# Kernel optimization log

Measured on AMD Instinct MI355X. Metric: run time of the kernel, lower is better.

## Reference

```python
import jax, jax.numpy as jnp
import numpy as np

GROUPS = 16
GROUP_SIZE = 16
K = 3
KK = K * K
BN_EPS = 1e-5


def setup_inputs() -> dict:
    key = jax.random.key(0)
    ks = jax.random.split(key, 6)
    B, C, H, W = 16, 256, 56, 56
    mid = C // 4  # rd_ratio = 4
    x = jax.random.normal(ks[0], (B, C, H, W), dtype=jnp.float32)
    w1 = jax.random.normal(ks[1], (mid, C), dtype=jnp.float32) * (1.0 / np.sqrt(C))
    bn_gamma = jnp.ones((mid,), dtype=jnp.float32)
    bn_beta = jnp.zeros((mid,), dtype=jnp.float32)
    bn_mean = jax.random.normal(ks[2], (mid,), dtype=jnp.float32) * 0.1
    bn_var = jax.random.uniform(ks[3], (mid,), dtype=jnp.float32, minval=0.5, maxval=1.5)
    w2 = jax.random.normal(ks[4], (KK * GROUPS, mid), dtype=jnp.float32) * (1.0 / np.sqrt(mid))
    b2 = jax.random.normal(ks[5], (KK * GROUPS,), dtype=jnp.float32) * 0.01
    return {"x": x, "w1": w1, "bn_gamma": bn_gamma, "bn_beta": bn_beta,
            "bn_mean": bn_mean, "bn_var": bn_var, "w2": w2, "b2": b2}


def reference(x, w1, bn_gamma, bn_beta, bn_mean, bn_var, w2, b2):
    B, C, H, W = x.shape
    # conv1: 1x1 conv + BatchNorm (eval) + ReLU
    t = jnp.einsum('bchw,oc->bohw', x, w1)
    scale = bn_gamma / jnp.sqrt(bn_var + BN_EPS)
    t = t * scale[None, :, None, None] + (bn_beta - bn_mean * scale)[None, :, None, None]
    t = jax.nn.relu(t)
    # conv2: 1x1 conv producing per-pixel kernels (B, KK*groups, H, W)
    weight = jnp.einsum('bchw,oc->bohw', t, w2) + b2[None, :, None, None]
    weight = weight.reshape(B, GROUPS, 1, KK, H, W)
    # unfold: extract 3x3 patches (pad=1, stride=1), kernel positions row-major
    xp = jnp.pad(x, ((0, 0), (0, 0), (1, 1), (1, 1)))
    patches = jnp.stack(
        [xp[:, :, i:i + H, j:j + W] for i in range(K) for j in range(K)],
        axis=2)  # (B, C, KK, H, W), matches torch unfold's (c*KK + kk) layout
    patches = patches.reshape(B, GROUPS, GROUP_SIZE, KK, H, W)
    out = (weight * patches).sum(axis=3).reshape(B, C, H, W)
    return out
```

## Files before the change

kernel.cpp:

```cpp
#include <hip/hip_runtime.h>


#define Cn    256
#define MID   64
#define Hn    56
#define Wn    56
#define HW    3136
#define Bn    16
#define NPIX  (Bn * HW)
#define CHW   (Cn * HW)
#define NKK   9
#define NG    16
#define GSZ   16
#define PXT   64
#define BN_EPS 1e-5f

#define GLOAD_LDS(src, dst, sz)                                                        \
  __builtin_amdgcn_global_load_lds(                                                    \
      (const __attribute__((address_space(1))) void*)(src),                            \
      (__attribute__((address_space(3))) void*)(dst), (sz), 0, 0)

__global__ __launch_bounds__(256) void prep_kernel(
    const float* __restrict__ w1,
    const float* __restrict__ gamma,
    const float* __restrict__ beta,
    const float* __restrict__ mean,
    const float* __restrict__ var,
    float* __restrict__ w1f,
    float* __restrict__ bias1) {
  int idx = blockIdx.x * 256 + threadIdx.x;
  if (idx < MID * Cn) {
    int c = idx >> 6;
    int o = idx & 63;
    float scale = gamma[o] / sqrtf(var[o] + BN_EPS);
    w1f[idx] = w1[o * Cn + c] * scale;
  } else if (idx < MID * Cn + MID) {
    int o = idx - MID * Cn;
    float scale = gamma[o] / sqrtf(var[o] + BN_EPS);
    bias1[o] = beta[o] - mean[o] * scale;
  }
}

__global__ __launch_bounds__(256) void conv1_kernel(
    const float* __restrict__ x,
    const float* __restrict__ w1f,
    const float* __restrict__ bias1,
    float* __restrict__ t) {
  __shared__ __align__(16) float lx[3][16][PXT];

  const int tid = threadIdx.x;
  const int px  = tid & 63;
  const int wv  = __builtin_amdgcn_readfirstlane(tid >> 6);

  const int bid = blockIdx.x;
  const int pc  = bid >> 1;
  const int oh  = bid & 1;
  const int px0 = pc * PXT;
  const int b   = px0 / HW;
  const int hw0 = px0 - b * HW;
  const float* xb = x + (size_t)b * CHW + hw0;

  const int rsub = px >> 4;
  const int csub = (px & 15) << 2;
  const int lrow = (wv << 2) + rsub;

  GLOAD_LDS(xb + (size_t)(lrow) * HW + csub, &lx[0][wv << 2][0], 16);
  GLOAD_LDS(xb + (size_t)(16 + lrow) * HW + csub, &lx[1][wv << 2][0], 16);

  float acc[8];
#pragma unroll
  for (int j = 0; j < 8; ++j) acc[j] = 0.0f;

  for (int k = 0; k < 16; ++k) {
    if (k < 15) {
      asm volatile("s_waitcnt vmcnt(1)" ::: "memory");
    } else {
      asm volatile("s_waitcnt vmcnt(0)" ::: "memory");
    }
    __builtin_amdgcn_s_barrier();
    __builtin_amdgcn_sched_barrier(0);
    if (k < 14) {
      const int nb = (k + 2) % 3;
      GLOAD_LDS(xb + (size_t)((k + 2) * 16 + lrow) * HW + csub,
                &lx[nb][wv << 2][0], 16);
    }
    const float* lxk = &lx[k % 3][0][0];
    const float* wr0 = w1f + (k << 10) + (oh << 5) + (wv << 3);
#pragma unroll
    for (int c = 0; c < 16; ++c) {
      const float xv = lxk[(c << 6) + px];
      const float* wr = wr0 + (c << 6);
      const float4 wa = *(const float4*)(wr + 0);
      const float4 wb = *(const float4*)(wr + 4);
      acc[0] = fmaf(xv, wa.x, acc[0]);
      acc[1] = fmaf(xv, wa.y, acc[1]);
      acc[2] = fmaf(xv, wa.z, acc[2]);
      acc[3] = fmaf(xv, wa.w, acc[3]);
      acc[4] = fmaf(xv, wb.x, acc[4]);
      acc[5] = fmaf(xv, wb.y, acc[5]);
      acc[6] = fmaf(xv, wb.z, acc[6]);
      acc[7] = fmaf(xv, wb.w, acc[7]);
    }
  }

#pragma unroll
  for (int j = 0; j < 8; ++j) {
    const int o = (oh << 5) + (wv << 3) + j;
    t[(size_t)o * NPIX + px0 + px] = fmaxf(acc[j] + bias1[o], 0.0f);
  }
}

#define LOADCH(dst, ch)                                                   \
  {                                                                       \
    const float* _xp = xcg + (size_t)(ch) * HW;                           \
    _Pragma("unroll")                                                     \
    for (int kk = 0; kk < NKK; ++kk) dst[kk] = _xp[off[kk]];              \
  }
#define CONSUME(src, ch)                                                  \
  {                                                                       \
    float s0 = wk[0] * src[0];                                            \
    float s1 = wk[1] * src[1];                                            \
    float s2 = wk[2] * src[2];                                            \
    s0 = fmaf(wk[3], src[3], s0);                                         \
    s1 = fmaf(wk[4], src[4], s1);                                         \
    s2 = fmaf(wk[5], src[5], s2);                                         \
    s0 = fmaf(wk[6], src[6], s0);                                         \
    s1 = fmaf(wk[7], src[7], s1);                                         \
    s2 = fmaf(wk[8], src[8], s2);                                         \
    ob[(size_t)(ch) * HW] = s0 + s1 + s2;                                 \
  }

__global__ __launch_bounds__(256, 4) void conv2_inv_kernel(
    const float* __restrict__ x,
    const float* __restrict__ t,
    const float* __restrict__ w2,
    const float* __restrict__ b2,
    float* __restrict__ out) {
  __shared__ __align__(16) float lt[MID][PXT];

  const int tid = threadIdx.x;
  const int px  = tid & 63;
  const int wv  = __builtin_amdgcn_readfirstlane(tid >> 6);

  const int bid = blockIdx.x;
  const int pc  = ((bid >> 5) << 3) + (bid & 7);
  const int gq  = (bid >> 3) & 3;
  const int g   = (gq << 2) + wv;

  const int px0 = pc * PXT;
  const int b   = px0 / HW;
  const int hw0 = px0 - b * HW;

  const int rsub = px >> 4;
  const int csub = (px & 15) << 2;

#pragma unroll
  for (int j = 0; j < 4; ++j) {
    const int r0 = (wv << 4) + (j << 2);
    GLOAD_LDS(t + (size_t)(r0 + rsub) * NPIX + px0 + csub, &lt[r0][0], 16);
  }

  const int hw = hw0 + px;
  const int h  = hw / Wn;
  const int w  = hw - h * Wn;

  int off[NKK];
  unsigned vmask = 0;
#pragma unroll
  for (int kk = 0; kk < NKK; ++kk) {
    const int di  = kk / 3 - 1;
    const int dj  = kk % 3 - 1;
    const int h2  = h + di;
    const int w2v = w + dj;
    const bool valid = ((unsigned)h2 < (unsigned)Hn) && ((unsigned)w2v < (unsigned)Wn);
    off[kk] = valid ? (h2 * Wn + w2v) : hw;
    vmask |= (valid ? 1u : 0u) << kk;
  }

  const float* xcg = x + (size_t)b * CHW + (size_t)(g * GSZ) * HW;
  float p0[NKK], p1[NKK], p2[NKK], p3[NKK];
  LOADCH(p0, 0)
  LOADCH(p1, 1)
  LOADCH(p2, 2)
  LOADCH(p3, 3)

  __syncthreads();

  float a[NKK];
#pragma unroll
  for (int kk = 0; kk < NKK; ++kk) a[kk] = b2[g * NKK + kk];

  const float* wg = w2 + (size_t)g * (NKK * MID);
#pragma unroll 4
  for (int o4 = 0; o4 < MID; o4 += 4) {
    const float t0 = lt[o4 + 0][px];
    const float t1 = lt[o4 + 1][px];
    const float t2 = lt[o4 + 2][px];
    const float t3 = lt[o4 + 3][px];
#pragma unroll
    for (int kk = 0; kk < NKK; ++kk) {
      const float4 w4 = *(const float4*)(wg + (kk << 6) + o4);
      a[kk] = fmaf(t3, w4.w, fmaf(t2, w4.z, fmaf(t1, w4.y, fmaf(t0, w4.x, a[kk]))));
    }
  }

  float wk[NKK];
#pragma unroll
  for (int kk = 0; kk < NKK; ++kk)
    wk[kk] = ((vmask >> kk) & 1u) ? a[kk] : 0.0f;

  float* ob = out + (size_t)b * CHW + (size_t)(g * GSZ) * HW + hw;

  CONSUME(p0, 0)  LOADCH(p0, 4)
  CONSUME(p1, 1)  LOADCH(p1, 5)
  CONSUME(p2, 2)  LOADCH(p2, 6)
  CONSUME(p3, 3)  LOADCH(p3, 7)
  CONSUME(p0, 4)  LOADCH(p0, 8)
  CONSUME(p1, 5)  LOADCH(p1, 9)
  CONSUME(p2, 6)  LOADCH(p2, 10)
  CONSUME(p3, 7)  LOADCH(p3, 11)
  CONSUME(p0, 8)  LOADCH(p0, 12)
  CONSUME(p1, 9)  LOADCH(p1, 13)
  CONSUME(p2, 10) LOADCH(p2, 14)
  CONSUME(p3, 11) LOADCH(p3, 15)
  CONSUME(p0, 12)
  CONSUME(p1, 13)
  CONSUME(p2, 14)
  CONSUME(p3, 15)
}

extern "C" void kernel_launch(void* const* d_in, const int* in_sizes, int n_in,
                              void* d_out, int out_size, void* d_ws, size_t ws_size,
                              hipStream_t stream) {
  const float* x     = (const float*)d_in[0];
  const float* w1    = (const float*)d_in[1];
  const float* gamma = (const float*)d_in[2];
  const float* beta  = (const float*)d_in[3];
  const float* mean  = (const float*)d_in[4];
  const float* var   = (const float*)d_in[5];
  const float* w2    = (const float*)d_in[6];
  const float* b2    = (const float*)d_in[7];
  float* out = (float*)d_out;

  char* ws = (char*)d_ws;
  float* t     = (float*)ws;
  float* w1f   = (float*)(ws + (size_t)MID * NPIX * 4);
  float* bias1 = (float*)(ws + (size_t)MID * NPIX * 4 + (size_t)MID * Cn * 4);

  prep_kernel<<<(MID * Cn + MID + 255) / 256, 256, 0, stream>>>(
      w1, gamma, beta, mean, var, w1f, bias1);
  conv1_kernel<<<NPIX / PXT * 2, 256, 0, stream>>>(x, w1f, bias1, t);
  conv2_inv_kernel<<<NPIX / PXT * 4, 256, 0, stream>>>(x, t, w2, b2, out);
}
```

Before: 161.1 us.

## Replace LDS staging with direct register loads in conv1 and conv2

```diff
diff --git a/kernel.cpp b/kernel.cpp
--- a/kernel.cpp
+++ b/kernel.cpp
@@ -14,11 +14,6 @@
 #define GSZ   16
 #define PXT   64
 #define BN_EPS 1e-5f
-
-#define GLOAD_LDS(src, dst, sz)                                                        \
-  __builtin_amdgcn_global_load_lds(                                                    \
-      (const __attribute__((address_space(1))) void*)(src),                            \
-      (__attribute__((address_space(3))) void*)(dst), (sz), 0, 0)
 
 __global__ __launch_bounds__(256) void prep_kernel(
     const float* __restrict__ w1,
@@ -46,8 +41,6 @@
     const float* __restrict__ w1f,
     const float* __restrict__ bias1,
     float* __restrict__ t) {
-  __shared__ __align__(16) float lx[3][16][PXT];
-
   const int tid = threadIdx.x;
   const int px  = tid & 63;
   const int wv  = __builtin_amdgcn_readfirstlane(tid >> 6);
@@ -58,48 +51,31 @@
   const int px0 = pc * PXT;
   const int b   = px0 / HW;
   const int hw0 = px0 - b * HW;
-  const float* xb = x + (size_t)b * CHW + hw0;
-
-  const int rsub = px >> 4;
-  const int csub = (px & 15) << 2;
-  const int lrow = (wv << 2) + rsub;
-
-  GLOAD_LDS(xb + (size_t)(lrow) * HW + csub, &lx[0][wv << 2][0], 16);
-  GLOAD_LDS(xb + (size_t)(16 + lrow) * HW + csub, &lx[1][wv << 2][0], 16);
+  const float* xb = x + (size_t)b * CHW + hw0 + px;
+
+  const float* wr0 = w1f + (oh << 5) + (wv << 3);
 
   float acc[8];
 #pragma unroll
   for (int j = 0; j < 8; ++j) acc[j] = 0.0f;
 
-  for (int k = 0; k < 16; ++k) {
-    if (k < 15) {
-      asm volatile("s_waitcnt vmcnt(1)" ::: "memory");
-    } else {
-      asm volatile("s_waitcnt vmcnt(0)" ::: "memory");
-    }
-    __builtin_amdgcn_s_barrier();
-    __builtin_amdgcn_sched_barrier(0);
-    if (k < 14) {
-      const int nb = (k + 2) % 3;
-      GLOAD_LDS(xb + (size_t)((k + 2) * 16 + lrow) * HW + csub,
-                &lx[nb][wv << 2][0], 16);
-    }
-    const float* lxk = &lx[k % 3][0][0];
-    const float* wr0 = w1f + (k << 10) + (oh << 5) + (wv << 3);
-#pragma unroll
-    for (int c = 0; c < 16; ++c) {
-      const float xv = lxk[(c << 6) + px];
-      const float* wr = wr0 + (c << 6);
+  for (int c = 0; c < Cn; c += 8) {
+    float xv[8];
+#pragma unroll
+    for (int i = 0; i < 8; ++i) xv[i] = xb[(size_t)(c + i) * HW];
+#pragma unroll
+    for (int i = 0; i < 8; ++i) {
+      const float* wr = wr0 + ((c + i) << 6);
       const float4 wa = *(const float4*)(wr + 0);
       const float4 wb = *(const float4*)(wr + 4);
-      acc[0] = fmaf(xv, wa.x, acc[0]);
-      acc[1] = fmaf(xv, wa.y, acc[1]);
-      acc[2] = fmaf(xv, wa.z, acc[2]);
-      acc[3] = fmaf(xv, wa.w, acc[3]);
-      acc[4] = fmaf(xv, wb.x, acc[4]);
-      acc[5] = fmaf(xv, wb.y, acc[5]);
-      acc[6] = fmaf(xv, wb.z, acc[6]);
-      acc[7] = fmaf(xv, wb.w, acc[7]);
+      acc[0] = fmaf(xv[i], wa.x, acc[0]);
+      acc[1] = fmaf(xv[i], wa.y, acc[1]);
+      acc[2] = fmaf(xv[i], wa.z, acc[2]);
+      acc[3] = fmaf(xv[i], wa.w, acc[3]);
+      acc[4] = fmaf(xv[i], wb.x, acc[4]);
+      acc[5] = fmaf(xv[i], wb.y, acc[5]);
+      acc[6] = fmaf(xv[i], wb.z, acc[6]);
+      acc[7] = fmaf(xv[i], wb.w, acc[7]);
     }
   }
 
@@ -129,36 +105,45 @@
     s2 = fmaf(wk[8], src[8], s2);                                         \
     ob[(size_t)(ch) * HW] = s0 + s1 + s2;                                 \
   }
-
-__global__ __launch_bounds__(256, 4) void conv2_inv_kernel(
+#define C2CHUNK(CUR, CH)                                                  \
+  {                                                                       \
+    _Pragma("unroll")                                                     \
+    for (int o4 = 0; o4 < 16; o4 += 4) {                                  \
+      const int ob_ = (CH) * 16 + o4;                                     \
+      _Pragma("unroll")                                                   \
+      for (int kk = 0; kk < NKK; ++kk) {                                  \
+        const float4 w4 = *(const float4*)(wg + (kk << 6) + ob_);         \
+        a[kk] = fmaf(CUR[o4 + 3], w4.w,                                   \
+                fmaf(CUR[o4 + 2], w4.z,                                   \
+                fmaf(CUR[o4 + 1], w4.y,                                   \
+                fmaf(CUR[o4 + 0], w4.x, a[kk]))));                        \
+      }                                                                   \
+    }                                                                     \
+  }
+
+__global__ __launch_bounds__(64) void conv2_inv_kernel(
     const float* __restrict__ x,
     const float* __restrict__ t,
     const float* __restrict__ w2,
     const float* __restrict__ b2,
     float* __restrict__ out) {
-  __shared__ __align__(16) float lt[MID][PXT];
-
-  const int tid = threadIdx.x;
-  const int px  = tid & 63;
-  const int wv  = __builtin_amdgcn_readfirstlane(tid >> 6);
+  const int px  = threadIdx.x;
 
   const int bid = blockIdx.x;
-  const int pc  = ((bid >> 5) << 3) + (bid & 7);
-  const int gq  = (bid >> 3) & 3;
-  const int g   = (gq << 2) + wv;
+  const int r   = bid & 7;
+  const int k   = bid >> 3;
+  const int g   = k & 15;
+  const int pc  = ((k >> 4) << 3) + r;
 
   const int px0 = pc * PXT;
   const int b   = px0 / HW;
   const int hw0 = px0 - b * HW;
 
-  const int rsub = px >> 4;
-  const int csub = (px & 15) << 2;
-
-#pragma unroll
-  for (int j = 0; j < 4; ++j) {
-    const int r0 = (wv << 4) + (j << 2);
-    GLOAD_LDS(t + (size_t)(r0 + rsub) * NPIX + px0 + csub, &lt[r0][0], 16);
-  }
+  const float* tb = t + px0 + px;
+
+  float tvA[16], tvB[16];
+#pragma unroll
+  for (int i = 0; i < 16; ++i) tvA[i] = tb[(size_t)i * NPIX];
 
   const int hw = hw0 + px;
   const int h  = hw / Wn;
@@ -177,39 +162,36 @@
     vmask |= (valid ? 1u : 0u) << kk;
   }
 
+  float a[NKK];
+#pragma unroll
+  for (int kk = 0; kk < NKK; ++kk) a[kk] = b2[g * NKK + kk];
+
+  const float* wg = w2 + (size_t)g * (NKK * MID);
+
+#pragma unroll
+  for (int i = 0; i < 16; ++i) tvB[i] = tb[(size_t)(16 + i) * NPIX];
+  C2CHUNK(tvA, 0)
+#pragma unroll
+  for (int i = 0; i < 16; ++i) tvA[i] = tb[(size_t)(32 + i) * NPIX];
+  C2CHUNK(tvB, 1)
+#pragma unroll
+  for (int i = 0; i < 16; ++i) tvB[i] = tb[(size_t)(48 + i) * NPIX];
+  C2CHUNK(tvA, 2)
+  C2CHUNK(tvB, 3)
+
+  float wk[NKK];
+#pragma unroll
+  for (int kk = 0; kk < NKK; ++kk)
+    wk[kk] = ((vmask >> kk) & 1u) ? a[kk] : 0.0f;
+
   const float* xcg = x + (size_t)b * CHW + (size_t)(g * GSZ) * HW;
+  float* ob = out + (size_t)b * CHW + (size_t)(g * GSZ) * HW + hw;
+
   float p0[NKK], p1[NKK], p2[NKK], p3[NKK];
   LOADCH(p0, 0)
   LOADCH(p1, 1)
   LOADCH(p2, 2)
   LOADCH(p3, 3)
-
-  __syncthreads();
-
-  float a[NKK];
-#pragma unroll
-  for (int kk = 0; kk < NKK; ++kk) a[kk] = b2[g * NKK + kk];
-
-  const float* wg = w2 + (size_t)g * (NKK * MID);
-#pragma unroll 4
-  for (int o4 = 0; o4 < MID; o4 += 4) {
-    const float t0 = lt[o4 + 0][px];
-    const float t1 = lt[o4 + 1][px];
-    const float t2 = lt[o4 + 2][px];
-    const float t3 = lt[o4 + 3][px];
-#pragma unroll
-    for (int kk = 0; kk < NKK; ++kk) {
-      const float4 w4 = *(const float4*)(wg + (kk << 6) + o4);
-      a[kk] = fmaf(t3, w4.w, fmaf(t2, w4.z, fmaf(t1, w4.y, fmaf(t0, w4.x, a[kk]))));
-    }
-  }
-
-  float wk[NKK];
-#pragma unroll
-  for (int kk = 0; kk < NKK; ++kk)
-    wk[kk] = ((vmask >> kk) & 1u) ? a[kk] : 0.0f;
-
-  float* ob = out + (size_t)b * CHW + (size_t)(g * GSZ) * HW + hw;
 
   CONSUME(p0, 0)  LOADCH(p0, 4)
   CONSUME(p1, 1)  LOADCH(p1, 5)
@@ -250,5 +232,5 @@
   prep_kernel<<<(MID * Cn + MID + 255) / 256, 256, 0, stream>>>(
       w1, gamma, beta, mean, var, w1f, bias1);
   conv1_kernel<<<NPIX / PXT * 2, 256, 0, stream>>>(x, w1f, bias1, t);
-  conv2_inv_kernel<<<NPIX / PXT * 4, 256, 0, stream>>>(x, t, w2, b2, out);
-}
+  conv2_inv_kernel<<<NPIX / PXT * NG, 64, 0, stream>>>(x, t, w2, b2, out);
+}
```

New measurement: 174.3 us. 1.08x slower.

## Split conv1 outputs into quarters and use buffer loads with OOB zeroing in conv2

Applied to the files above, without the earlier changes.

```diff
diff --git a/kernel.cpp b/kernel.cpp
--- a/kernel.cpp
+++ b/kernel.cpp
@@ -19,6 +19,11 @@
   __builtin_amdgcn_global_load_lds(                                                    \
       (const __attribute__((address_space(1))) void*)(src),                            \
       (__attribute__((address_space(3))) void*)(dst), (sz), 0, 0)
+
+static __device__ __forceinline__ __amdgpu_buffer_rsrc_t
+make_rsrc(const void* p, unsigned bytes) {
+  return __builtin_amdgcn_make_buffer_rsrc((void*)p, (short)0, (int)bytes, 0x20000);
+}
 
 __global__ __launch_bounds__(256) void prep_kernel(
     const float* __restrict__ w1,
@@ -53,8 +58,10 @@
   const int wv  = __builtin_amdgcn_readfirstlane(tid >> 6);
 
   const int bid = blockIdx.x;
-  const int pc  = bid >> 1;
-  const int oh  = bid & 1;
+  const int r   = bid & 7;
+  const int k0  = bid >> 3;
+  const int oq  = k0 & 3;
+  const int pc  = ((k0 >> 2) << 3) + r;
   const int px0 = pc * PXT;
   const int b   = px0 / HW;
   const int hw0 = px0 - b * HW;
@@ -64,12 +71,10 @@
   const int csub = (px & 15) << 2;
   const int lrow = (wv << 2) + rsub;
 
-  GLOAD_LDS(xb + (size_t)(lrow) * HW + csub, &lx[0][wv << 2][0], 16);
+  GLOAD_LDS(xb + (size_t)lrow * HW + csub, &lx[0][wv << 2][0], 16);
   GLOAD_LDS(xb + (size_t)(16 + lrow) * HW + csub, &lx[1][wv << 2][0], 16);
 
-  float acc[8];
-#pragma unroll
-  for (int j = 0; j < 8; ++j) acc[j] = 0.0f;
+  float acc[4] = {0.0f, 0.0f, 0.0f, 0.0f};
 
   for (int k = 0; k < 16; ++k) {
     if (k < 15) {
@@ -85,36 +90,31 @@
                 &lx[nb][wv << 2][0], 16);
     }
     const float* lxk = &lx[k % 3][0][0];
-    const float* wr0 = w1f + (k << 10) + (oh << 5) + (wv << 3);
+    const float* wr0 = w1f + (k << 10) + (oq << 4) + (wv << 2);
 #pragma unroll
     for (int c = 0; c < 16; ++c) {
       const float xv = lxk[(c << 6) + px];
-      const float* wr = wr0 + (c << 6);
-      const float4 wa = *(const float4*)(wr + 0);
-      const float4 wb = *(const float4*)(wr + 4);
+      const float4 wa = *(const float4*)(wr0 + (c << 6));
       acc[0] = fmaf(xv, wa.x, acc[0]);
       acc[1] = fmaf(xv, wa.y, acc[1]);
       acc[2] = fmaf(xv, wa.z, acc[2]);
       acc[3] = fmaf(xv, wa.w, acc[3]);
-      acc[4] = fmaf(xv, wb.x, acc[4]);
-      acc[5] = fmaf(xv, wb.y, acc[5]);
-      acc[6] = fmaf(xv, wb.z, acc[6]);
-      acc[7] = fmaf(xv, wb.w, acc[7]);
-    }
-  }
-
-#pragma unroll
-  for (int j = 0; j < 8; ++j) {
-    const int o = (oh << 5) + (wv << 3) + j;
+    }
+  }
+
+#pragma unroll
+  for (int j = 0; j < 4; ++j) {
+    const int o = (oq << 4) + (wv << 2) + j;
     t[(size_t)o * NPIX + px0 + px] = fmaxf(acc[j] + bias1[o], 0.0f);
   }
 }
 
 #define LOADCH(dst, ch)                                                   \
   {                                                                       \
-    const float* _xp = xcg + (size_t)(ch) * HW;                           \
     _Pragma("unroll")                                                     \
-    for (int kk = 0; kk < NKK; ++kk) dst[kk] = _xp[off[kk]];              \
+    for (int kk = 0; kk < NKK; ++kk)                                      \
+      dst[kk] = __int_as_float(__builtin_amdgcn_raw_buffer_load_b32(      \
+          xrs, voff[kk], (ch) * (HW * 4), 0));                            \
   }
 #define CONSUME(src, ch)                                                  \
   {                                                                       \
@@ -127,7 +127,8 @@
     s0 = fmaf(wk[6], src[6], s0);                                         \
     s1 = fmaf(wk[7], src[7], s1);                                         \
     s2 = fmaf(wk[8], src[8], s2);                                         \
-    ob[(size_t)(ch) * HW] = s0 + s1 + s2;                                 \
+    __builtin_amdgcn_raw_buffer_store_b32(__float_as_int(s0 + s1 + s2),   \
+                                          ors, hw4, (ch) * (HW * 4), 0); \
   }
 
 __global__ __launch_bounds__(256, 4) void conv2_inv_kernel(
@@ -160,12 +161,17 @@
     GLOAD_LDS(t + (size_t)(r0 + rsub) * NPIX + px0 + csub, &lt[r0][0], 16);
   }
 
+  const __amdgpu_buffer_rsrc_t xrs =
+      make_rsrc(x + (size_t)b * CHW + (size_t)(g * GSZ) * HW, GSZ * HW * 4);
+  const __amdgpu_buffer_rsrc_t ors =
+      make_rsrc(out + (size_t)b * CHW + (size_t)(g * GSZ) * HW, GSZ * HW * 4);
+
   const int hw = hw0 + px;
   const int h  = hw / Wn;
   const int w  = hw - h * Wn;
-
-  int off[NKK];
-  unsigned vmask = 0;
+  const int hw4 = hw << 2;
+
+  int voff[NKK];
 #pragma unroll
   for (int kk = 0; kk < NKK; ++kk) {
     const int di  = kk / 3 - 1;
@@ -173,12 +179,12 @@
     const int h2  = h + di;
     const int w2v = w + dj;
     const bool valid = ((unsigned)h2 < (unsigned)Hn) && ((unsigned)w2v < (unsigned)Wn);
-    off[kk] = valid ? (h2 * Wn + w2v) : hw;
-    vmask |= (valid ? 1u : 0u) << kk;
-  }
-
-  const float* xcg = x + (size_t)b * CHW + (size_t)(g * GSZ) * HW;
+    voff[kk] = valid ? ((h2 * Wn + w2v) << 2) : 0x60000000;
+  }
+
   float p0[NKK], p1[NKK], p2[NKK], p3[NKK];
+  float wkdummy[1];
+  (void)wkdummy;
   LOADCH(p0, 0)
   LOADCH(p1, 1)
   LOADCH(p2, 2)
@@ -204,12 +210,7 @@
     }
   }
 
-  float wk[NKK];
-#pragma unroll
-  for (int kk = 0; kk < NKK; ++kk)
-    wk[kk] = ((vmask >> kk) & 1u) ? a[kk] : 0.0f;
-
-  float* ob = out + (size_t)b * CHW + (size_t)(g * GSZ) * HW + hw;
+  const float* wk = a;
 
   CONSUME(p0, 0)  LOADCH(p0, 4)
   CONSUME(p1, 1)  LOADCH(p1, 5)
@@ -249,6 +250,6 @@
 
   prep_kernel<<<(MID * Cn + MID + 255) / 256, 256, 0, stream>>>(
       w1, gamma, beta, mean, var, w1f, bias1);
-  conv1_kernel<<<NPIX / PXT * 2, 256, 0, stream>>>(x, w1f, bias1, t);
+  conv1_kernel<<<NPIX / PXT * 4, 256, 0, stream>>>(x, w1f, bias1, t);
   conv2_inv_kernel<<<NPIX / PXT * 4, 256, 0, stream>>>(x, t, w2, b2, out);
 }
```

After: 165.9 us. 1.03x slower.
